# Kernel optimization log

Measured on AMD Instinct MI355X. Metric: run time of the kernel, lower is better.

## Reference

```python
import jax, jax.numpy as jnp
import numpy as np

IN_F, OUT_F, R = 4096, 4096, 16
ALPHA = 32.0
SCALING = ALPHA / R


def setup_inputs() -> dict:
    key = jax.random.key(0)
    kx, kw, ka = jax.random.split(key, 3)
    x = jax.random.normal(kx, (4, 2048, IN_F), dtype=jnp.float32)
    # xavier_normal for weight: std = sqrt(2/(fan_in+fan_out))
    std = float(np.sqrt(2.0 / (IN_F + OUT_F)))
    weight = jax.random.normal(kw, (OUT_F, IN_F), dtype=jnp.float32) * std
    bias = jnp.zeros((OUT_F,), dtype=jnp.float32)
    A = jax.random.normal(ka, (R, IN_F), dtype=jnp.float32) * 0.01
    # B initialized to zeros in the module, but use small random values so the
    # LoRA path is numerically exercised for kernel correctness testing.
    B = jax.random.normal(jax.random.fold_in(key, 7), (OUT_F, R), dtype=jnp.float32) * 0.01
    return {"x": x, "weight": weight, "bias": bias, "A": A, "B": B}


def reference(x, weight, bias, A, B):
    # out = x @ W^T + bias + scaling * ((x @ A^T) @ B^T)
    out = jnp.einsum('bsi,oi->bso', x, weight) + bias
    xa = jnp.einsum('bsi,ri->bsr', x, A)           # [b, s, r] low-rank projection
    out = out + SCALING * jnp.einsum('bsr,or->bso', xa, B)
    return out
```

## Files before the change

### kernel.cpp

```cpp
#include <hip/hip_runtime.h>
#include <hip/hip_bf16.h>
#include <cstdint>
#include <cstddef>


#define IN_F   4096
#define OUT_F  4096
#define MROWS  8192
#define RLORA  16
#define LORA_SCALE 2.0f

#define CAST_BLOCKS 32768
#define FOLD_BLOCKS 4096

#define BM   256
#define BN   256
#define BKT  32
#define NT   (IN_F / BKT)

typedef __bf16 bf16x8 __attribute__((ext_vector_type(8)));
typedef float  f32x4  __attribute__((ext_vector_type(4)));
typedef int    i32x4  __attribute__((ext_vector_type(4)));

__device__ __forceinline__ unsigned short f2bf_rne(float f) {
    union { float f; unsigned u; } v; v.f = f;
    unsigned u = v.u;
    return (unsigned short)((u + 0x7FFFu + ((u >> 16) & 1u)) >> 16);
}

__device__ __forceinline__ void gl_lds16(const unsigned short* g, unsigned short* l) {
    __builtin_amdgcn_global_load_lds(
        (const __attribute__((address_space(1))) unsigned int*)g,
        (__attribute__((address_space(3))) unsigned int*)l,
        16, 0, 0);
}


__global__ void prep_kernel(const float* __restrict__ x,
                            const float* __restrict__ W,
                            const float* __restrict__ A,
                            const float* __restrict__ B,
                            unsigned short* __restrict__ xb,
                            unsigned short* __restrict__ wb) {
    __shared__ float sB[RLORA];
    const int bid = blockIdx.x;
    if (bid < CAST_BLOCKS) {
        int i = bid * blockDim.x + threadIdx.x;
        float4 v = ((const float4*)x)[i];
        ushort4 o;
        o.x = f2bf_rne(v.x); o.y = f2bf_rne(v.y);
        o.z = f2bf_rne(v.z); o.w = f2bf_rne(v.w);
        ((ushort4*)xb)[i] = o;
    } else {
        const int o = bid - CAST_BLOCKS;
        if (threadIdx.x < RLORA) sB[threadIdx.x] = B[o * RLORA + threadIdx.x];
        __syncthreads();
        const float4* W4  = (const float4*)(W + (size_t)o * IN_F);
        ushort4*      Wp4 = (ushort4*)(wb + (size_t)o * IN_F);
        for (int i4 = threadIdx.x; i4 < IN_F / 4; i4 += blockDim.x) {
            float4 w = W4[i4];
            float ax = 0.f, ay = 0.f, az = 0.f, aw = 0.f;
            #pragma unroll
            for (int r = 0; r < RLORA; ++r) {
                float4 a = ((const float4*)(A + (size_t)r * IN_F))[i4];
                float s = sB[r];
                ax += s * a.x; ay += s * a.y; az += s * a.z; aw += s * a.w;
            }
            w.x += LORA_SCALE * ax; w.y += LORA_SCALE * ay;
            w.z += LORA_SCALE * az; w.w += LORA_SCALE * aw;
            ushort4 ov;
            ov.x = f2bf_rne(w.x); ov.y = f2bf_rne(w.y);
            ov.z = f2bf_rne(w.z); ov.w = f2bf_rne(w.w);
            Wp4[i4] = ov;
        }
    }
}


__global__ __launch_bounds__(512, 2)
void gemm_bt_bias(const unsigned short* __restrict__ Xb,
                  const unsigned short* __restrict__ Wb,
                  const float* __restrict__ bias,
                  float* __restrict__ out) {
    __shared__ __align__(16) unsigned short smem[4 * 16384];

    const int tid  = threadIdx.x;
    const int wave = tid >> 6;
    const int lane = tid & 63;
    const int quad = lane >> 4;
    const int r16  = lane & 15;
    const int wm   = wave >> 2;
    const int wn   = wave & 3;

    const int bid = blockIdx.x;
    const int xcd = bid & 7;
    const int t   = bid >> 3;
    const int n0  = (xcd * 2 + (t & 1)) * BN;
    const int m0  = (t >> 1) * BM;

    const int q0  = wave * 128 + lane;
    const int q1  = q0 + 64;
    const int r0  = q0 >> 2, k0c = (q0 & 3) ^ ((r0 >> 1) & 3);
    const int r1  = q1 >> 2, k1c = (q1 & 3) ^ ((r1 >> 1) & 3);

    const unsigned short* gA0 = Xb + (size_t)(m0 + r0) * IN_F + k0c * 8;
    const unsigned short* gA1 = Xb + (size_t)(m0 + r1) * IN_F + k1c * 8;
    const unsigned short* gB0 = Wb + (size_t)(n0 + r0) * IN_F + k0c * 8;
    const unsigned short* gB1 = Wb + (size_t)(n0 + r1) * IN_F + k1c * 8;

    unsigned short* const lA0 = smem + wave * 1024;
    unsigned short* const lA1 = lA0 + 512;
    unsigned short* const lB0 = smem + 8192 + wave * 1024;
    unsigned short* const lB1 = lB0 + 512;

    const unsigned slot  = (unsigned)(quad ^ ((r16 >> 1) & 3));
    const unsigned aoff  = (unsigned)((wm * 128 + r16) * 64) + slot * 16;
    const unsigned boff  = 16384u + (unsigned)((wn * 64 + r16) * 64) + slot * 16;
    const unsigned sbase = (unsigned)(size_t)
        ((__attribute__((address_space(3))) unsigned short*)smem);

    f32x4 acc[8][4] = {};

#define STAGE_A(TILE) {                                                  \
    const unsigned off = (unsigned)(((TILE) & 3) << 14);                 \
    gl_lds16(gA0, lA0 + off); gl_lds16(gA1, lA1 + off);                  \
    gA0 += BKT; gA1 += BKT; }
#define STAGE_B(TILE) {                                                  \
    const unsigned off = (unsigned)(((TILE) & 3) << 14);                 \
    gl_lds16(gB0, lB0 + off); gl_lds16(gB1, lB1 + off);                  \
    gB0 += BKT; gB1 += BKT; }

    STAGE_A(0) STAGE_B(0)
    STAGE_A(1) STAGE_B(1)
    STAGE_A(2) STAGE_B(2)
    asm volatile("s_waitcnt vmcnt(8)" ::: "memory");
    __builtin_amdgcn_s_barrier();

    for (int p = 0; p < NT; ++p) {
        const unsigned bufb = sbase + ((unsigned)(p & 3) << 15);
        const unsigned ab = bufb + aoff;
        const unsigned bb = bufb + boff;

        i32x4 aR[4], bR[4], aS[4];
        asm volatile("ds_read_b128 %0, %1"             : "=v"(bR[0]) : "v"(bb));
        asm volatile("ds_read_b128 %0, %1 offset:1024" : "=v"(bR[1]) : "v"(bb));
        asm volatile("ds_read_b128 %0, %1 offset:2048" : "=v"(bR[2]) : "v"(bb));
        asm volatile("ds_read_b128 %0, %1 offset:3072" : "=v"(bR[3]) : "v"(bb));
        asm volatile("ds_read_b128 %0, %1"             : "=v"(aR[0]) : "v"(ab));
        asm volatile("ds_read_b128 %0, %1 offset:1024" : "=v"(aR[1]) : "v"(ab));
        asm volatile("ds_read_b128 %0, %1 offset:2048" : "=v"(aR[2]) : "v"(ab));
        asm volatile("ds_read_b128 %0, %1 offset:3072" : "=v"(aR[3]) : "v"(ab));
        if (p + 3 < NT) STAGE_A(p + 3)
        __builtin_amdgcn_s_barrier();
        asm volatile("s_waitcnt lgkmcnt(0)" ::: "memory");
        __builtin_amdgcn_sched_barrier(0);
        __builtin_amdgcn_s_setprio(1);
        #pragma unroll
        for (int mi = 0; mi < 4; ++mi) {
            const bf16x8 a = __builtin_bit_cast(bf16x8, aR[mi]);
            #pragma unroll
            for (int nj = 0; nj < 4; ++nj)
                acc[mi][nj] = __builtin_amdgcn_mfma_f32_16x16x32_bf16(
                    a, __builtin_bit_cast(bf16x8, bR[nj]), acc[mi][nj], 0, 0, 0);
        }
        __builtin_amdgcn_sched_barrier(0);
        __builtin_amdgcn_s_setprio(0);
        __builtin_amdgcn_s_barrier();

        asm volatile("ds_read_b128 %0, %1 offset:4096" : "=v"(aS[0]) : "v"(ab));
        asm volatile("ds_read_b128 %0, %1 offset:5120" : "=v"(aS[1]) : "v"(ab));
        asm volatile("ds_read_b128 %0, %1 offset:6144" : "=v"(aS[2]) : "v"(ab));
        asm volatile("ds_read_b128 %0, %1 offset:7168" : "=v"(aS[3]) : "v"(ab));
        if (p + 3 < NT) STAGE_B(p + 3)
        __builtin_amdgcn_s_barrier();
        asm volatile("s_waitcnt lgkmcnt(0)" ::: "memory");
        __builtin_amdgcn_sched_barrier(0);
        __builtin_amdgcn_s_setprio(1);
        #pragma unroll
        for (int mi = 0; mi < 4; ++mi) {
            const bf16x8 a = __builtin_bit_cast(bf16x8, aS[mi]);
            #pragma unroll
            for (int nj = 0; nj < 4; ++nj)
                acc[mi + 4][nj] = __builtin_amdgcn_mfma_f32_16x16x32_bf16(
                    a, __builtin_bit_cast(bf16x8, bR[nj]), acc[mi + 4][nj], 0, 0, 0);
        }
        __builtin_amdgcn_sched_barrier(0);
        __builtin_amdgcn_s_setprio(0);
        if (p + 3 < NT)       { asm volatile("s_waitcnt vmcnt(8)" ::: "memory"); }
        else if (p + 3 == NT) { asm volatile("s_waitcnt vmcnt(4)" ::: "memory"); }
        else                  { asm volatile("s_waitcnt vmcnt(0)" ::: "memory"); }
        __builtin_amdgcn_s_barrier();
    }
#undef STAGE_A
#undef STAGE_B

    float bv[4];
    #pragma unroll
    for (int nj = 0; nj < 4; ++nj)
        bv[nj] = bias[n0 + wn * 64 + nj * 16 + r16];

    #pragma unroll
    for (int mi = 0; mi < 8; ++mi) {
        #pragma unroll
        for (int i = 0; i < 4; ++i) {
            const int mg = m0 + wm * 128 + mi * 16 + quad * 4 + i;
            float* orow = out + (size_t)mg * OUT_F + (n0 + wn * 64 + r16);
            #pragma unroll
            for (int nj = 0; nj < 4; ++nj)
                orow[nj * 16] = acc[mi][nj][i] + bv[nj];
        }
    }
}


extern "C" void kernel_launch(void* const* d_in, const int* in_sizes, int n_in,
                              void* d_out, int out_size, void* d_ws, size_t ws_size,
                              hipStream_t stream) {
    const float* x    = (const float*)d_in[0];
    const float* W    = (const float*)d_in[1];
    const float* bias = (const float*)d_in[2];
    const float* A    = (const float*)d_in[3];
    const float* B    = (const float*)d_in[4];
    float* out = (float*)d_out;

    unsigned short* xb = (unsigned short*)d_ws;
    unsigned short* wb = xb + (size_t)MROWS * IN_F;

    prep_kernel<<<CAST_BLOCKS + FOLD_BLOCKS, 256, 0, stream>>>(x, W, A, B, xb, wb);
    gemm_bt_bias<<<(MROWS / BM) * (OUT_F / BN), 512, 0, stream>>>(xb, wb, bias, out);
}
```

Before: 549.1 us.

## Double-buffer LDS fragment reads in registers and prefetch next tile during MFMA

Restructures the K loop into a two-tile unrolled ping-pong where the LDS fragment reads for the next K tile are issued before the current tile's MFMA clusters run, using two register sets (even/odd). Global-to-LDS staging of A and B is merged into one stage per tile, and the loop now has one barrier per tile instead of four. The aim is to hide LDS read latency behind matrix-core work and cut synchronisation. In exchange it uses roughly twice the fragment registers, which may hurt occupancy or cause spills, and the tighter LDS buffer reuse with fewer barriers is riskier to get right.

```diff
diff --git a/kernel.cpp b/kernel.cpp
--- a/kernel.cpp
+++ b/kernel.cpp
@@ -120,79 +120,114 @@
         ((__attribute__((address_space(3))) unsigned short*)smem);
 
     f32x4 acc[8][4] = {};
-
-#define STAGE_A(TILE) {                                                  \
+    i32x4 aE[8], bE[4], aO[8], bO[4];
+
+#define STAGE(TILE) {                                                    \
     const unsigned off = (unsigned)(((TILE) & 3) << 14);                 \
     gl_lds16(gA0, lA0 + off); gl_lds16(gA1, lA1 + off);                  \
-    gA0 += BKT; gA1 += BKT; }
-#define STAGE_B(TILE) {                                                  \
-    const unsigned off = (unsigned)(((TILE) & 3) << 14);                 \
     gl_lds16(gB0, lB0 + off); gl_lds16(gB1, lB1 + off);                  \
-    gB0 += BKT; gB1 += BKT; }
-
-    STAGE_A(0) STAGE_B(0)
-    STAGE_A(1) STAGE_B(1)
-    STAGE_A(2) STAGE_B(2)
-    asm volatile("s_waitcnt vmcnt(8)" ::: "memory");
+    gA0 += BKT; gA1 += BKT; gB0 += BKT; gB1 += BKT; }
+
+#define RD_LO(AV, BV, S) {                                               \
+    const unsigned bufb_ = sbase + ((unsigned)((S) & 3) << 15);          \
+    const unsigned ab_ = bufb_ + aoff, bb_ = bufb_ + boff;               \
+    asm volatile("ds_read_b128 %0, %1"             : "=v"(BV[0]) : "v"(bb_)); \
+    asm volatile("ds_read_b128 %0, %1 offset:1024" : "=v"(BV[1]) : "v"(bb_)); \
+    asm volatile("ds_read_b128 %0, %1 offset:2048" : "=v"(BV[2]) : "v"(bb_)); \
+    asm volatile("ds_read_b128 %0, %1 offset:3072" : "=v"(BV[3]) : "v"(bb_)); \
+    asm volatile("ds_read_b128 %0, %1"             : "=v"(AV[0]) : "v"(ab_)); \
+    asm volatile("ds_read_b128 %0, %1 offset:1024" : "=v"(AV[1]) : "v"(ab_)); \
+    asm volatile("ds_read_b128 %0, %1 offset:2048" : "=v"(AV[2]) : "v"(ab_)); \
+    asm volatile("ds_read_b128 %0, %1 offset:3072" : "=v"(AV[3]) : "v"(ab_)); }
+
+#define RD_HI(AV, S) {                                                   \
+    const unsigned bufb_ = sbase + ((unsigned)((S) & 3) << 15);          \
+    const unsigned ab_ = bufb_ + aoff;                                   \
+    asm volatile("ds_read_b128 %0, %1 offset:4096" : "=v"(AV[4]) : "v"(ab_)); \
+    asm volatile("ds_read_b128 %0, %1 offset:5120" : "=v"(AV[5]) : "v"(ab_)); \
+    asm volatile("ds_read_b128 %0, %1 offset:6144" : "=v"(AV[6]) : "v"(ab_)); \
+    asm volatile("ds_read_b128 %0, %1 offset:7168" : "=v"(AV[7]) : "v"(ab_)); }
+
+#define CLUSTER(AV, BV, MLO, MHI) {                                      \
+    _Pragma("unroll")                                                    \
+    for (int mi = MLO; mi < MHI; ++mi) {                                 \
+        const bf16x8 a_ = __builtin_bit_cast(bf16x8, AV[mi]);            \
+        _Pragma("unroll")                                                \
+        for (int nj = 0; nj < 4; ++nj)                                   \
+            acc[mi][nj] = __builtin_amdgcn_mfma_f32_16x16x32_bf16(       \
+                a_, __builtin_bit_cast(bf16x8, BV[nj]), acc[mi][nj], 0, 0, 0); \
+    } }
+
+    STAGE(0) STAGE(1) STAGE(2)
+    asm volatile("s_waitcnt vmcnt(4)" ::: "memory");
     __builtin_amdgcn_s_barrier();
-
-    for (int p = 0; p < NT; ++p) {
-        const unsigned bufb = sbase + ((unsigned)(p & 3) << 15);
-        const unsigned ab = bufb + aoff;
-        const unsigned bb = bufb + boff;
-
-        i32x4 aR[4], bR[4], aS[4];
-        asm volatile("ds_read_b128 %0, %1"             : "=v"(bR[0]) : "v"(bb));
-        asm volatile("ds_read_b128 %0, %1 offset:1024" : "=v"(bR[1]) : "v"(bb));
-        asm volatile("ds_read_b128 %0, %1 offset:2048" : "=v"(bR[2]) : "v"(bb));
-        asm volatile("ds_read_b128 %0, %1 offset:3072" : "=v"(bR[3]) : "v"(bb));
-        asm volatile("ds_read_b128 %0, %1"             : "=v"(aR[0]) : "v"(ab));
-        asm volatile("ds_read_b128 %0, %1 offset:1024" : "=v"(aR[1]) : "v"(ab));
-        asm volatile("ds_read_b128 %0, %1 offset:2048" : "=v"(aR[2]) : "v"(ab));
-        asm volatile("ds_read_b128 %0, %1 offset:3072" : "=v"(aR[3]) : "v"(ab));
-        if (p + 3 < NT) STAGE_A(p + 3)
+    RD_LO(aE, bE, 0)
+    asm volatile("s_waitcnt lgkmcnt(0)" ::: "memory");
+    __builtin_amdgcn_sched_barrier(0);
+
+    for (int p = 0; p < NT - 2; p += 2) {
+        RD_HI(aE, p)
+        RD_LO(aO, bO, p + 1)
+        STAGE(p + 3)
+        __builtin_amdgcn_sched_barrier(0);
+        __builtin_amdgcn_s_setprio(1);
+        CLUSTER(aE, bE, 0, 4)
+        asm volatile("s_waitcnt lgkmcnt(8)" ::: "memory");
+        __builtin_amdgcn_sched_barrier(0);
+        CLUSTER(aE, bE, 4, 8)
+        __builtin_amdgcn_s_setprio(0);
+        __builtin_amdgcn_sched_barrier(0);
+        asm volatile("s_waitcnt lgkmcnt(0)" ::: "memory");
+        __builtin_amdgcn_sched_barrier(0);
+        asm volatile("s_waitcnt vmcnt(4)" ::: "memory");
         __builtin_amdgcn_s_barrier();
+
+        RD_HI(aO, p + 1)
+        RD_LO(aE, bE, p + 2)
+        if (p + 4 < NT) STAGE(p + 4)
+        __builtin_amdgcn_sched_barrier(0);
+        __builtin_amdgcn_s_setprio(1);
+        CLUSTER(aO, bO, 0, 4)
+        asm volatile("s_waitcnt lgkmcnt(8)" ::: "memory");
+        __builtin_amdgcn_sched_barrier(0);
+        CLUSTER(aO, bO, 4, 8)
+        __builtin_amdgcn_s_setprio(0);
+        __builtin_amdgcn_sched_barrier(0);
         asm volatile("s_waitcnt lgkmcnt(0)" ::: "memory");
         __builtin_amdgcn_sched_barrier(0);
-        __builtin_amdgcn_s_setprio(1);
-        #pragma unroll
-        for (int mi = 0; mi < 4; ++mi) {
-            const bf16x8 a = __builtin_bit_cast(bf16x8, aR[mi]);
-            #pragma unroll
-            for (int nj = 0; nj < 4; ++nj)
-                acc[mi][nj] = __builtin_amdgcn_mfma_f32_16x16x32_bf16(
-                    a, __builtin_bit_cast(bf16x8, bR[nj]), acc[mi][nj], 0, 0, 0);
-        }
-        __builtin_amdgcn_sched_barrier(0);
-        __builtin_amdgcn_s_setprio(0);
-        __builtin_amdgcn_s_barrier();
-
-        asm volatile("ds_read_b128 %0, %1 offset:4096" : "=v"(aS[0]) : "v"(ab));
-        asm volatile("ds_read_b128 %0, %1 offset:5120" : "=v"(aS[1]) : "v"(ab));
-        asm volatile("ds_read_b128 %0, %1 offset:6144" : "=v"(aS[2]) : "v"(ab));
-        asm volatile("ds_read_b128 %0, %1 offset:7168" : "=v"(aS[3]) : "v"(ab));
-        if (p + 3 < NT) STAGE_B(p + 3)
-        __builtin_amdgcn_s_barrier();
-        asm volatile("s_waitcnt lgkmcnt(0)" ::: "memory");
-        __builtin_amdgcn_sched_barrier(0);
-        __builtin_amdgcn_s_setprio(1);
-        #pragma unroll
-        for (int mi = 0; mi < 4; ++mi) {
-            const bf16x8 a = __builtin_bit_cast(bf16x8, aS[mi]);
-            #pragma unroll
-            for (int nj = 0; nj < 4; ++nj)
-                acc[mi + 4][nj] = __builtin_amdgcn_mfma_f32_16x16x32_bf16(
-                    a, __builtin_bit_cast(bf16x8, bR[nj]), acc[mi + 4][nj], 0, 0, 0);
-        }
-        __builtin_amdgcn_sched_barrier(0);
-        __builtin_amdgcn_s_setprio(0);
-        if (p + 3 < NT)       { asm volatile("s_waitcnt vmcnt(8)" ::: "memory"); }
-        else if (p + 3 == NT) { asm volatile("s_waitcnt vmcnt(4)" ::: "memory"); }
-        else                  { asm volatile("s_waitcnt vmcnt(0)" ::: "memory"); }
+        if (p + 4 < NT) { asm volatile("s_waitcnt vmcnt(4)" ::: "memory"); }
+        else            { asm volatile("s_waitcnt vmcnt(0)" ::: "memory"); }
         __builtin_amdgcn_s_barrier();
     }
-#undef STAGE_A
-#undef STAGE_B
+
+    RD_HI(aE, NT - 2)
+    RD_LO(aO, bO, NT - 1)
+    __builtin_amdgcn_sched_barrier(0);
+    __builtin_amdgcn_s_setprio(1);
+    CLUSTER(aE, bE, 0, 4)
+    asm volatile("s_waitcnt lgkmcnt(8)" ::: "memory");
+    __builtin_amdgcn_sched_barrier(0);
+    CLUSTER(aE, bE, 4, 8)
+    __builtin_amdgcn_s_setprio(0);
+    __builtin_amdgcn_sched_barrier(0);
+    asm volatile("s_waitcnt lgkmcnt(0)" ::: "memory");
+    __builtin_amdgcn_sched_barrier(0);
+    asm volatile("s_waitcnt vmcnt(0)" ::: "memory");
+    __builtin_amdgcn_s_barrier();
+
+    RD_HI(aO, NT - 1)
+    __builtin_amdgcn_sched_barrier(0);
+    __builtin_amdgcn_s_setprio(1);
+    CLUSTER(aO, bO, 0, 4)
+    asm volatile("s_waitcnt lgkmcnt(0)" ::: "memory");
+    __builtin_amdgcn_sched_barrier(0);
+    CLUSTER(aO, bO, 4, 8)
+    __builtin_amdgcn_s_setprio(0);
+
+#undef STAGE
+#undef RD_LO
+#undef RD_HI
+#undef CLUSTER
 
     float bv[4];
     #pragma unroll
```

Result: faster. 531.2 us (-3.3%).
